# Performance work log

Hardware: AMD Instinct MI355X
Metric: run time of the kernel (lower is better)

Reference implementation:

```python
import jax, jax.numpy as jnp
import numpy as np

K = 3  # kernel size -> n_qubits = K*K, but only qubit 0 affects PauliZ(0) expval

def setup_inputs() -> dict:
    key = jax.random.key(0)
    k1, k2 = jax.random.split(key)
    x = jax.random.uniform(k1, (64, 1, 512, 512), dtype=jnp.float32)
    weight = jax.random.normal(k2, (K * K,), dtype=jnp.float32)
    threshold = jnp.zeros((1,), dtype=jnp.float32)
    return {"x": x, "weight": weight, "threshold": threshold}

def reference(x, weight, threshold):
    # Quantum circuit math: |0> -RY(pi*x0)-RY(w0)-> <Z> = cos(pi*x0 + w0).
    # Patch's flattened element 0 is the top-left pixel x[b,0,i,j].
    b, _, h, w = x.shape
    out_h, out_w = h - K + 1, w - K + 1
    top_left = x[:, 0, :out_h, :out_w]                      # [B, H', W']
    conv = jnp.cos(jnp.pi * top_left + weight[0])           # qnode expval per patch
    out = jax.nn.sigmoid(conv - threshold[0])               # shared threshold
    return out[:, None, :, :]                               # stack over 1 kernel size
```

## Files before the change

### kernel.cpp

```cpp
#include <hip/hip_runtime.h>


#define BATCH 64
#define H_IN 512
#define W_IN 512
#define H_OUT 510
#define W_OUT 510
#define W_OUT_V2 (W_OUT / 2)

__global__ void __launch_bounds__(256) conv154_kernel(
        const float* __restrict__ x,
        const float* __restrict__ weight,
        const float* __restrict__ threshold,
        float* __restrict__ out) {
    const float w0  = weight[0];
    const float thr = threshold[0];
    const float PI  = 3.14159265358979323846f;

    const int total = BATCH * H_OUT * W_OUT_V2;
    const int stride = gridDim.x * blockDim.x;
    for (int idx = blockIdx.x * blockDim.x + threadIdx.x; idx < total; idx += stride) {
        const int j2 = idx % W_OUT_V2;
        const int t  = idx / W_OUT_V2;
        const int i  = t % H_OUT;
        const int b  = t / H_OUT;

        const size_t in_off  = (size_t)b * (H_IN * W_IN)   + (size_t)i * W_IN  + j2 * 2;
        const size_t out_off = (size_t)b * (H_OUT * W_OUT) + (size_t)i * W_OUT + j2 * 2;

        const float2 v = *reinterpret_cast<const float2*>(x + in_off);

        float2 r;
        const float c0 = __cosf(fmaf(v.x, PI, w0));
        const float c1 = __cosf(fmaf(v.y, PI, w0));
        r.x = 1.0f / (1.0f + __expf(thr - c0));
        r.y = 1.0f / (1.0f + __expf(thr - c1));

        *reinterpret_cast<float2*>(out + out_off) = r;
    }
}

extern "C" void kernel_launch(void* const* d_in, const int* in_sizes, int n_in,
                              void* d_out, int out_size, void* d_ws, size_t ws_size,
                              hipStream_t stream) {
    const float* x   = (const float*)d_in[0];
    const float* w   = (const float*)d_in[1];
    const float* thr = (const float*)d_in[2];
    float* out       = (float*)d_out;

    const int total  = BATCH * H_OUT * W_OUT_V2;
    const int block  = 256;
    int grid = (total + block - 1) / block;
    if (grid > 4096) grid = 4096;
    conv154_kernel<<<grid, block, 0, stream>>>(x, w, thr, out);
}
```

Baseline: 119.6 us.

## Map blocks to output rows with float4 loads and fast reciprocal

```diff
diff --git a/kernel.cpp b/kernel.cpp
--- a/kernel.cpp
+++ b/kernel.cpp
@@ -6,7 +6,10 @@
 #define W_IN 512
 #define H_OUT 510
 #define W_OUT 510
-#define W_OUT_V2 (W_OUT / 2)
+#define ROWS_TOTAL (BATCH * H_OUT)
+#define ROWS_PER_BLOCK 2
+
+struct f4 { float x, y, z, w; };
 
 __global__ void __launch_bounds__(256) conv154_kernel(
         const float* __restrict__ x,
@@ -17,27 +20,30 @@
     const float thr = threshold[0];
     const float PI  = 3.14159265358979323846f;
 
-    const int total = BATCH * H_OUT * W_OUT_V2;
-    const int stride = gridDim.x * blockDim.x;
-    for (int idx = blockIdx.x * blockDim.x + threadIdx.x; idx < total; idx += stride) {
-        const int j2 = idx % W_OUT_V2;
-        const int t  = idx / W_OUT_V2;
-        const int i  = t % H_OUT;
-        const int b  = t / H_OUT;
+    const int t   = threadIdx.x;
+    const int row = blockIdx.x * ROWS_PER_BLOCK + (t >> 7);
+    const int j   = t & 127;
+    int col = j * 4;
+    if (col > W_OUT - 4) col = W_OUT - 4;
 
-        const size_t in_off  = (size_t)b * (H_IN * W_IN)   + (size_t)i * W_IN  + j2 * 2;
-        const size_t out_off = (size_t)b * (H_OUT * W_OUT) + (size_t)i * W_OUT + j2 * 2;
+    const int b = row / H_OUT;
+    const int i = row - b * H_OUT;
 
-        const float2 v = *reinterpret_cast<const float2*>(x + in_off);
+    const float* in_p  = x   + (size_t)b * (H_IN * W_IN) + (size_t)i * W_IN + col;
+    float*       out_p = out + (size_t)row * W_OUT + col;
 
-        float2 r;
-        const float c0 = __cosf(fmaf(v.x, PI, w0));
-        const float c1 = __cosf(fmaf(v.y, PI, w0));
-        r.x = 1.0f / (1.0f + __expf(thr - c0));
-        r.y = 1.0f / (1.0f + __expf(thr - c1));
+    const f4 v = *reinterpret_cast<const f4*>(in_p);
 
-        *reinterpret_cast<float2*>(out + out_off) = r;
+    f4 r;
+    #pragma unroll
+    for (int k = 0; k < 4; ++k) {
+        const float xv = (&v.x)[k];
+        const float c  = __cosf(fmaf(xv, PI, w0));
+        const float e  = __expf(thr - c);
+        (&r.x)[k] = __builtin_amdgcn_rcpf(1.0f + e);
     }
+
+    *reinterpret_cast<f4*>(out_p) = r;
 }
 
 extern "C" void kernel_launch(void* const* d_in, const int* in_sizes, int n_in,
@@ -48,9 +54,6 @@
     const float* thr = (const float*)d_in[2];
     float* out       = (float*)d_out;
 
-    const int total  = BATCH * H_OUT * W_OUT_V2;
-    const int block  = 256;
-    int grid = (total + block - 1) / block;
-    if (grid > 4096) grid = 4096;
-    conv154_kernel<<<grid, block, 0, stream>>>(x, w, thr, out);
+    const int grid = ROWS_TOTAL / ROWS_PER_BLOCK;
+    conv154_kernel<<<grid, 256, 0, stream>>>(x, w, thr, out);
 }
```

New measurement: 112.8 us. 1.06x faster.
